# Performance work log

Hardware: AMD Instinct MI355X
Metric: run time of the kernel (lower is better)

## Reference

```python
import jax, jax.numpy as jnp
import numpy as np

N = 2048      # global node count (num_global_nodes)
K = 8         # number of clients
NK = 1024     # local nodes per client
TAU_C = 0.5
GAMMA = 1.0
TAU_S = 0.5


def setup_inputs() -> dict:
    key = jax.random.key(0)
    k1, k2 = jax.random.split(key)
    # local adjacencies in [0,1) so thresholds tau_c/tau_s are meaningful
    client_adj = jax.random.uniform(k1, (K, NK, NK), dtype=jnp.float32)
    # per-client global node ids: sorted, duplicate-free subset of range(N)
    perm_keys = jax.random.split(k2, K)
    perms = jax.vmap(lambda k: jax.random.permutation(k, N)[:NK])(perm_keys)
    client_idx = jnp.sort(perms, axis=1).astype(jnp.int32)
    return {"client_adj": client_adj, "client_idx": client_idx}


def reference(client_adj, client_idx):
    # client_adj: [K, Nk, Nk] float, client_idx: [K, Nk] int
    Kc = client_adj.shape[0]
    dt = client_adj.dtype
    karr = jnp.arange(Kc)[:, None, None]           # [K,1,1]
    ix = client_idx[:, :, None]                    # [K,Nk,1] row ids (meshgrid 'ij')
    iy = client_idx[:, None, :]                    # [K,1,Nk] col ids

    # scatter each client's local adjacency into the common node space
    A_stack = jnp.zeros((Kc, N, N), dt).at[karr, ix, iy].set(client_adj)  # [K,N,N]
    mask = jnp.zeros((Kc, N, N), dt).at[karr, ix, iy].set(jnp.ones_like(client_adj))

    num_obs = jnp.maximum(mask.sum(axis=0), 1e-5)                 # [N,N]
    A_mean = (A_stack * mask).sum(axis=0) / num_obs               # consensus mean
    C = ((A_stack > TAU_C).astype(dt) * mask).sum(axis=0) / num_obs  # consensus rate
    V = (((A_stack - A_mean[None]) ** 2) * mask).sum(axis=0) / num_obs  # variance
    S = C * jnp.exp(-GAMMA * V)                                   # invariance score
    M_inv = (S > TAU_S).astype(dt)
    A_inv = M_inv * A_mean * (num_obs > 1e-5).astype(dt)
    return A_inv
```

## Files before the change

### kernel.cpp

```cpp
#include <hip/hip_runtime.h>
#include <math.h>

#define N  2048
#define K  8
#define NK 1024
#define R  4
#define TPB 512
#define SLOT NK
#define TAU_C 0.5f
#define TAU_S 0.5f

__global__ void __launch_bounds__(TPB, 4)
fia_fused(const float* __restrict__ adj,
          const int*   __restrict__ idx,
          float* __restrict__ out) {
    __shared__ short  jj[K][N];
    __shared__ short  ixs[K][R];
    __shared__ float  stage[K][NK + 4];
    __shared__ float  lutCS[81];
    __shared__ float2 lutB[81];
    __shared__ float  lutR[16];

    const int tid = threadIdx.x;
    const int X0  = blockIdx.x * R;

    {
        int4  m1 = make_int4(-1, -1, -1, -1);
        int4* p4 = (int4*)&jj[0][0];
        #pragma unroll
        for (int q = 0; q < (K * N * 2) / (16 * TPB); ++q)
            p4[q * TPB + tid] = m1;
        if (tid < K * R) ((short*)ixs)[tid] = (short)-1;
        if (tid < K) stage[tid][SLOT] = 0.0f;
        if (tid < 16) lutR[tid] = 1.0f / fmaxf((float)tid, 1e-5f);
        if (tid < 81) {
            int cn = tid / 9, cc = tid % 9;
            float nn = fmaxf((float)cn, 1e-5f);
            float C  = (float)cc / nn;
            lutCS[tid] = C;
            float lo, hi;
            if (2 * cc <= cn) { lo = -2.0f; hi = -1.0f; }
            else {
                float B = logf(2.0f * C);
                float d = 1e-3f * (1.0f + fabsf(B));
                lo = (B - d) * (float)cn;
                hi = (B + d) * (float)cn;
            }
            lutB[tid] = make_float2(lo, hi);
        }
    }
    __syncthreads();

    #pragma unroll
    for (int it = 0; it < (K * NK) / (4 * TPB); ++it) {
        int  t4   = it * TPB + tid;
        int4 w    = ((const int4*)idx)[t4];
        int  base = t4 * 4;
        int  k    = base >> 10;
        int  p    = base & (NK - 1);
        jj[k][w.x] = (short)(p);
        jj[k][w.y] = (short)(p + 1);
        jj[k][w.z] = (short)(p + 2);
        jj[k][w.w] = (short)(p + 3);
        int r0 = w.x - X0, r1 = w.y - X0, r2 = w.z - X0, r3 = w.w - X0;
        if ((unsigned)r0 < (unsigned)R) ixs[k][r0] = (short)(p);
        if ((unsigned)r1 < (unsigned)R) ixs[k][r1] = (short)(p + 1);
        if ((unsigned)r2 < (unsigned)R) ixs[k][r2] = (short)(p + 2);
        if ((unsigned)r3 < (unsigned)R) ixs[k][r3] = (short)(p + 3);
    }
    __syncthreads();

    const int y0 = tid * 4;
    int jc[K][4];
    int jmask[4] = {0, 0, 0, 0};
    #pragma unroll
    for (int k = 0; k < K; ++k) {
        short4 v = *(const short4*)&jj[k][y0];
        int j0 = v.x, j1 = v.y, j2 = v.z, j3 = v.w;
        jmask[0] |= (j0 >= 0) ? (1 << k) : 0;
        jmask[1] |= (j1 >= 0) ? (1 << k) : 0;
        jmask[2] |= (j2 >= 0) ? (1 << k) : 0;
        jmask[3] |= (j3 >= 0) ? (1 << k) : 0;
        jc[k][0] = (j0 >= 0) ? j0 : SLOT;
        jc[k][1] = (j1 >= 0) ? j1 : SLOT;
        jc[k][2] = (j2 >= 0) ? j2 : SLOT;
        jc[k][3] = (j3 >= 0) ? j3 : SLOT;
    }

    #pragma unroll 1
    for (int r = 0; r < R; ++r) {
        int kp = 0;
        int ixr[K];
        #pragma unroll
        for (int k = 0; k < K; ++k) {
            int v = (int)ixs[k][r];
            ixr[k] = __builtin_amdgcn_readfirstlane(v);
            kp |= (ixr[k] >= 0) ? (1 << k) : 0;
        }

        float2 sr[K];
        #pragma unroll
        for (int k = 0; k < K; ++k) {
            if (ixr[k] >= 0) {
                const float2* __restrict__ src =
                    (const float2*)(adj + ((size_t)k * NK + (size_t)ixr[k]) * NK);
                sr[k] = src[tid];
            }
        }
        __syncthreads();
        #pragma unroll
        for (int k = 0; k < K; ++k) {
            if (ixr[k] >= 0)
                ((float2*)&stage[k][0])[tid] = sr[k];
        }
        __syncthreads();

        float sum[4]   = {0.f, 0.f, 0.f, 0.f};
        float sumsq[4] = {0.f, 0.f, 0.f, 0.f};
        int   csi[4]   = {0, 0, 0, 0};
        #pragma unroll
        for (int k = 0; k < K; ++k) {
            if ((kp >> k) & 1) {
                #pragma unroll
                for (int yy = 0; yy < 4; ++yy) {
                    float a = stage[k][jc[k][yy]];
                    sum[yy]   += a;
                    sumsq[yy]  = fmaf(a, a, sumsq[yy]);
                    csi[yy]   += (a > TAU_C) ? 1 : 0;
                }
            }
        }

        float res[4];
        #pragma unroll
        for (int yy = 0; yy < 4; ++yy) {
            const int m   = jmask[yy] & kp;
            const int cnt = __popc(m);
            const float cf = (float)cnt;
            float mean = sum[yy] * lutR[cnt];
            float t    = fmaf(cf, mean, -2.0f * sum[yy]);
            float vsf  = fmaf(mean, t, sumsq[yy]);

            const int li = cnt * 9 + csi[yy];
            float2 bb = lutB[li];
            float rr;
            if (__builtin_expect(vsf >= bb.x && vsf <= bb.y, 0)) {
                float n      = fmaxf(cf, 1e-5f);
                float mean_e = sum[yy] / n;
                float vs = 0.f;
                #pragma unroll
                for (int k = 0; k < K; ++k) {
                    if ((kp >> k) & 1) {
                        bool  p = (m >> k) & 1;
                        float a = stage[k][jc[k][yy]];
                        float d = a - mean_e;
                        vs += p ? d * d : 0.f;
                    }
                }
                float C = lutCS[li];
                float V = vs / n;
                float S = C * expf(-V);
                rr = (S > TAU_S && cnt > 0) ? mean_e : 0.f;
            } else {
                rr = (vsf < bb.x) ? mean : 0.f;
            }
            res[yy] = rr;
        }

        float4 o;
        o.x = res[0]; o.y = res[1]; o.z = res[2]; o.w = res[3];
        *(float4*)(out + (size_t)(X0 + r) * N + y0) = o;
    }
}

extern "C" void kernel_launch(void* const* d_in, const int* in_sizes, int n_in,
                              void* d_out, int out_size, void* d_ws, size_t ws_size,
                              hipStream_t stream) {
    const float* adj = (const float*)d_in[0];
    const int*   idx = (const int*)d_in[1];
    float*       out = (float*)d_out;

    dim3 block(TPB, 1, 1);
    dim3 grid(N / R, 1, 1);
    fia_fused<<<grid, block, 0, stream>>>(adj, idx, out);
}
```

Measured before the change: 19.65 us.

## Double-buffer staged adjacency rows to overlap next-row loads with compute

Replaces the per-row loop with an unrolled software pipeline using two shared staging buffers, one of which aliases the jj index table after it is consumed. Global loads for row r+1 are issued before computing row r and written to the alternate buffer afterward, with sched_barriers to keep that ordering. This removes one of the two __syncthreads per row and hides global load latency behind the LDS reduction. In exchange it needs more live registers to hold the prefetched rows and an extra barrier before the jj region is reused.

Measured after the change: 21.42 us. 1.09x slower.

```diff
diff --git a/kernel.cpp b/kernel.cpp
--- a/kernel.cpp
+++ b/kernel.cpp
@@ -10,13 +10,109 @@
 #define TAU_C 0.5f
 #define TAU_S 0.5f
 
+
+#define ROW_PASS(rr, CUR)                                                      \
+    {                                                                          \
+        int kpC = 0;                                                           \
+        _Pragma("unroll")                                                      \
+        for (int k = 0; k < K; ++k) {                                          \
+            int v_ = (int)ixs[k][rr];                                          \
+            kpC |= (__builtin_amdgcn_readfirstlane(v_) >= 0) ? (1 << k) : 0;   \
+        }                                                                      \
+        float sum[4]   = {0.f, 0.f, 0.f, 0.f};                                 \
+        float sumsq[4] = {0.f, 0.f, 0.f, 0.f};                                 \
+        int   csi[4]   = {0, 0, 0, 0};                                         \
+        _Pragma("unroll")                                                      \
+        for (int k = 0; k < K; ++k) {                                          \
+            if ((kpC >> k) & 1) {                             \
+                _Pragma("unroll")                                              \
+                for (int yy = 0; yy < 4; ++yy) {                               \
+                    float a = CUR[k][jc[k][yy]];              \
+                    sum[yy]   += a;                    \
+                    sumsq[yy]  = fmaf(a, a, sumsq[yy]);                        \
+                    csi[yy]   += (a > TAU_C) ? 1 : 0;                          \
+                }                                                              \
+            }                                                                  \
+        }                                                                      \
+        float res[4];                                                          \
+        _Pragma("unroll")                                                      \
+        for (int yy = 0; yy < 4; ++yy) {                                       \
+            const int m   = jmask[yy] & kpC;                                   \
+            const int cnt = __popc(m);                                         \
+            const float cf = (float)cnt;                                       \
+            float mean = sum[yy] * lutR[cnt];           \
+            float t    = fmaf(cf, mean, -2.0f * sum[yy]);                      \
+            float vsf  = fmaf(mean, t, sumsq[yy]);        \
+            const int li = cnt * 9 + csi[yy];                                  \
+            float2 bb = lutB[li];                                              \
+            float rr_;                                                         \
+            if (__builtin_expect(vsf >= bb.x && vsf <= bb.y, 0)) {             \
+                float n      = fmaxf(cf, 1e-5f);                               \
+                float mean_e = sum[yy] / n;                   \
+                float vs = 0.f;                                                \
+                _Pragma("unroll")                                              \
+                for (int k = 0; k < K; ++k) {                                  \
+                    if ((kpC >> k) & 1) {                                      \
+                        bool  p = (m >> k) & 1;                                \
+                        float a = CUR[k][jc[k][yy]];                           \
+                        float d = a - mean_e;                                  \
+                        vs += p ? d * d : 0.f;          \
+                    }                                                          \
+                }                                                              \
+                float C = lutCS[li];                    \
+                float V = vs / n;                             \
+                float S = C * expf(-V);                      \
+                rr_ = (S > TAU_S && cnt > 0) ? mean_e : 0.f;                   \
+            } else {                                                           \
+                rr_ = (vsf < bb.x) ? mean : 0.f;          \
+            }                                                                  \
+            res[yy] = rr_;                                                     \
+        }                                                                      \
+        float4 o_;                                                             \
+        o_.x = res[0]; o_.y = res[1]; o_.z = res[2]; o_.w = res[3];            \
+        *(float4*)(out + (size_t)(X0 + (rr)) * N + y0) = o_;                   \
+    }
+
+#define ROW_STEP(rr, CUR, NXT)                                                 \
+    {                                                                          \
+        int kpN = 0, ixN_[K];                                                  \
+        _Pragma("unroll")                                                      \
+        for (int k = 0; k < K; ++k) {                                          \
+            int v_ = (int)ixs[k][(rr) + 1];                                    \
+            ixN_[k] = __builtin_amdgcn_readfirstlane(v_);                      \
+            kpN |= (ixN_[k] >= 0) ? (1 << k) : 0;                              \
+        }                                                                      \
+        float2 sr[K];                                                          \
+        _Pragma("unroll")                                                      \
+        for (int k = 0; k < K; ++k) {                                          \
+            if ((kpN >> k) & 1) {                             \
+                const float2* __restrict__ src_ =                              \
+                    (const float2*)(adj + ((size_t)k * NK +                    \
+                                           (size_t)ixN_[k]) * NK);             \
+                sr[k] = src_[tid];                           \
+            }                                                                  \
+        }                                                                      \
+        __builtin_amdgcn_sched_barrier(0);               \
+        ROW_PASS(rr, CUR)                                                      \
+        __builtin_amdgcn_sched_barrier(0);              \
+        _Pragma("unroll")                                                      \
+        for (int k = 0; k < K; ++k) {                                          \
+            if ((kpN >> k) & 1)                                                \
+                ((float2*)&NXT[k][0])[tid] = sr[k];       \
+        }                                                                      \
+        __syncthreads();                                      \
+    }
+
 __global__ void __launch_bounds__(TPB, 4)
 fia_fused(const float* __restrict__ adj,
           const int*   __restrict__ idx,
           float* __restrict__ out) {
-    __shared__ short  jj[K][N];
+    __shared__ float stA[K][NK + 4];
+    __shared__ union {
+        short jj[K][N];
+        float stB[K][NK + 4];
+    } u;
     __shared__ short  ixs[K][R];
-    __shared__ float  stage[K][NK + 4];
     __shared__ float  lutCS[81];
     __shared__ float2 lutB[81];
     __shared__ float  lutR[16];
@@ -26,12 +122,12 @@
 
     {
         int4  m1 = make_int4(-1, -1, -1, -1);
-        int4* p4 = (int4*)&jj[0][0];
+        int4* p4 = (int4*)&u.jj[0][0];
         #pragma unroll
         for (int q = 0; q < (K * N * 2) / (16 * TPB); ++q)
             p4[q * TPB + tid] = m1;
         if (tid < K * R) ((short*)ixs)[tid] = (short)-1;
-        if (tid < K) stage[tid][SLOT] = 0.0f;
+        if (tid < K) stA[tid][SLOT] = 0.0f;
         if (tid < 16) lutR[tid] = 1.0f / fmaxf((float)tid, 1e-5f);
         if (tid < 81) {
             int cn = tid / 9, cc = tid % 9;
@@ -58,10 +154,10 @@
         int  base = t4 * 4;
         int  k    = base >> 10;
         int  p    = base & (NK - 1);
-        jj[k][w.x] = (short)(p);
-        jj[k][w.y] = (short)(p + 1);
-        jj[k][w.z] = (short)(p + 2);
-        jj[k][w.w] = (short)(p + 3);
+        u.jj[k][w.x] = (short)(p);
+        u.jj[k][w.y] = (short)(p + 1);
+        u.jj[k][w.z] = (short)(p + 2);
+        u.jj[k][w.w] = (short)(p + 3);
         int r0 = w.x - X0, r1 = w.y - X0, r2 = w.z - X0, r3 = w.w - X0;
         if ((unsigned)r0 < (unsigned)R) ixs[k][r0] = (short)(p);
         if ((unsigned)r1 < (unsigned)R) ixs[k][r1] = (short)(p + 1);
@@ -75,7 +171,7 @@
     int jmask[4] = {0, 0, 0, 0};
     #pragma unroll
     for (int k = 0; k < K; ++k) {
-        short4 v = *(const short4*)&jj[k][y0];
+        short4 v = *(const short4*)&u.jj[k][y0];
         int j0 = v.x, j1 = v.y, j2 = v.z, j3 = v.w;
         jmask[0] |= (j0 >= 0) ? (1 << k) : 0;
         jmask[1] |= (j1 >= 0) ? (1 << k) : 0;
@@ -86,91 +182,38 @@
         jc[k][2] = (j2 >= 0) ? j2 : SLOT;
         jc[k][3] = (j3 >= 0) ? j3 : SLOT;
     }
-
-    #pragma unroll 1
-    for (int r = 0; r < R; ++r) {
-        int kp = 0;
-        int ixr[K];
+    __syncthreads();
+
+    if (tid < K) u.stB[tid][SLOT] = 0.0f;
+    {
+        int kp0 = 0, ix0[K];
         #pragma unroll
         for (int k = 0; k < K; ++k) {
-            int v = (int)ixs[k][r];
-            ixr[k] = __builtin_amdgcn_readfirstlane(v);
-            kp |= (ixr[k] >= 0) ? (1 << k) : 0;
-        }
-
-        float2 sr[K];
+            int v = (int)ixs[k][0];
+            ix0[k] = __builtin_amdgcn_readfirstlane(v);
+            kp0 |= (ix0[k] >= 0) ? (1 << k) : 0;
+        }
+        float2 s0[K];
         #pragma unroll
         for (int k = 0; k < K; ++k) {
-            if (ixr[k] >= 0) {
+            if ((kp0 >> k) & 1) {
                 const float2* __restrict__ src =
-                    (const float2*)(adj + ((size_t)k * NK + (size_t)ixr[k]) * NK);
-                sr[k] = src[tid];
+                    (const float2*)(adj + ((size_t)k * NK + (size_t)ix0[k]) * NK);
+                s0[k] = src[tid];
             }
         }
+        #pragma unroll
+        for (int k = 0; k < K; ++k) {
+            if ((kp0 >> k) & 1)
+                ((float2*)&stA[k][0])[tid] = s0[k];
+        }
         __syncthreads();
-        #pragma unroll
-        for (int k = 0; k < K; ++k) {
-            if (ixr[k] >= 0)
-                ((float2*)&stage[k][0])[tid] = sr[k];
-        }
-        __syncthreads();
-
-        float sum[4]   = {0.f, 0.f, 0.f, 0.f};
-        float sumsq[4] = {0.f, 0.f, 0.f, 0.f};
-        int   csi[4]   = {0, 0, 0, 0};
-        #pragma unroll
-        for (int k = 0; k < K; ++k) {
-            if ((kp >> k) & 1) {
-                #pragma unroll
-                for (int yy = 0; yy < 4; ++yy) {
-                    float a = stage[k][jc[k][yy]];
-                    sum[yy]   += a;
-                    sumsq[yy]  = fmaf(a, a, sumsq[yy]);
-                    csi[yy]   += (a > TAU_C) ? 1 : 0;
-                }
-            }
-        }
-
-        float res[4];
-        #pragma unroll
-        for (int yy = 0; yy < 4; ++yy) {
-            const int m   = jmask[yy] & kp;
-            const int cnt = __popc(m);
-            const float cf = (float)cnt;
-            float mean = sum[yy] * lutR[cnt];
-            float t    = fmaf(cf, mean, -2.0f * sum[yy]);
-            float vsf  = fmaf(mean, t, sumsq[yy]);
-
-            const int li = cnt * 9 + csi[yy];
-            float2 bb = lutB[li];
-            float rr;
-            if (__builtin_expect(vsf >= bb.x && vsf <= bb.y, 0)) {
-                float n      = fmaxf(cf, 1e-5f);
-                float mean_e = sum[yy] / n;
-                float vs = 0.f;
-                #pragma unroll
-                for (int k = 0; k < K; ++k) {
-                    if ((kp >> k) & 1) {
-                        bool  p = (m >> k) & 1;
-                        float a = stage[k][jc[k][yy]];
-                        float d = a - mean_e;
-                        vs += p ? d * d : 0.f;
-                    }
-                }
-                float C = lutCS[li];
-                float V = vs / n;
-                float S = C * expf(-V);
-                rr = (S > TAU_S && cnt > 0) ? mean_e : 0.f;
-            } else {
-                rr = (vsf < bb.x) ? mean : 0.f;
-            }
-            res[yy] = rr;
-        }
-
-        float4 o;
-        o.x = res[0]; o.y = res[1]; o.z = res[2]; o.w = res[3];
-        *(float4*)(out + (size_t)(X0 + r) * N + y0) = o;
-    }
+    }
+
+    ROW_STEP(0, stA,   u.stB)
+    ROW_STEP(1, u.stB, stA)
+    ROW_STEP(2, stA,   u.stB)
+    ROW_PASS(3, u.stB)
 }
 
 extern "C" void kernel_launch(void* const* d_in, const int* in_sizes, int n_in,
```
